# Performance work log

Hardware: AMD Instinct MI355X
Metric: run time of the kernel (lower is better)

## Reference

```python
import jax, jax.numpy as jnp
import numpy as np

PRECS = 1e-05
# HBV parameter scaling bounds (order: BETA, FC, K0, K1, K2, LP, PERC, UZL, TT, CFMAX, CFR, CWH, BETAET)
LB = jnp.array([1.0, 50.0, 0.05, 0.01, 0.001, 0.2, 0.0, 0.0, -2.5, 0.5, 0.0, 0.0, 0.3], dtype=jnp.float32)
UB = jnp.array([6.0, 1000.0, 0.9, 0.5, 0.2, 1.0, 10.0, 100.0, 2.5, 10.0, 0.1, 0.2, 5.0], dtype=jnp.float32)

NSTEP, NGRID, MU = 730, 1000, 8

def setup_inputs() -> dict:
    key = jax.random.key(0)
    k1, k2, k3, k4 = jax.random.split(key, 4)
    P = jax.random.uniform(k1, (NSTEP, NGRID), jnp.float32) * 10.0      # precip mm/day
    T = jax.random.normal(k2, (NSTEP, NGRID), jnp.float32) * 8.0 + 2.0  # temp degC
    ET = jax.random.uniform(k3, (NSTEP, NGRID), jnp.float32) * 5.0      # PET mm/day
    x = jnp.stack([P, T, ET], axis=-1)                                   # [Nstep, Ngrid, 3]
    parameters = jax.random.uniform(k4, (NSTEP, NGRID, 13, MU), jnp.float32)  # raw in [0,1]
    tdlst = jnp.arange(2, dtype=jnp.int32)  # -> param indices {12, 0} = BETAET, BETA dynamic
    return {"x": x, "parameters": parameters, "staind": NSTEP - 1, "tdlst": tdlst, "mu": MU}

def _hbv_forward(x, parameters, staind, tdlst):
    # scale raw params to physical ranges: [Nstep, Ngrid, 13, mu]
    parT = LB[None, None, :, None] + parameters * (UB - LB)[None, None, :, None]
    # static params taken from time index staind, broadcast over time
    parhbv = jnp.broadcast_to(parT[staind][None], parT.shape)
    # dynamic params: dydrop=0 -> bernoulli mask is all zeros -> comPar = dynPar
    idx = jnp.mod(jnp.asarray(tdlst) - 1, 13)
    parhbv = parhbv.at[:, :, idx, :].set(parT[:, :, idx, :])

    Ngrid = x.shape[1]
    mu = parameters.shape[-1]
    init = tuple(jnp.full((Ngrid, mu), 0.001, dtype=jnp.float32) for _ in range(5))

    def step(carry, inp):
        SP, MW, SM, SUZ, SLZ = carry
        P_, T_, ET_, par = inp              # P_/T_/ET_: [Ngrid], par: [Ngrid, 13, mu]
        P_, T_, ET_ = P_[:, None], T_[:, None], ET_[:, None]
        BETA, FC, K0, K1, K2, LP, PERCc, UZL, TT, CFMAX, CFR, CWH, BETAET = (
            par[:, i] for i in range(13))
        is_rain = (T_ >= TT).astype(jnp.float32)
        RAIN = P_ * is_rain
        SNOW = P_ * (1.0 - is_rain)
        SP = SP + SNOW
        melt = jnp.minimum(jnp.maximum(CFMAX * (T_ - TT), 0.0), SP)
        MW = MW + melt
        SP = SP - melt
        refr = jnp.minimum(jnp.maximum(CFR * CFMAX * (TT - T_), 0.0), MW)
        SP = SP + refr
        MW = MW - refr
        tosoil = jnp.maximum(MW - CWH * SP, 0.0)
        MW = MW - tosoil
        soil_wetness = jnp.clip((SM / FC) ** BETA, 0.0, 1.0)
        recharge = (RAIN + tosoil) * soil_wetness
        SM = SM + RAIN + tosoil - recharge
        excess = jnp.maximum(SM - FC, 0.0)
        SM = SM - excess
        evapfactor = jnp.clip((SM / (LP * FC)) ** BETAET, 0.0, 1.0)
        ETact = jnp.minimum(SM, ET_ * evapfactor)
        SM = jnp.maximum(SM - ETact, PRECS)
        SUZ = SUZ + recharge + excess
        PERC = jnp.minimum(SUZ, PERCc)
        SUZ = SUZ - PERC
        Q0 = K0 * jnp.maximum(SUZ - UZL, 0.0)
        SUZ = SUZ - Q0
        Q1 = K1 * SUZ
        SUZ = SUZ - Q1
        SLZ = SLZ + PERC
        Q2 = K2 * SLZ
        SLZ = SLZ - Q2
        return (SP, MW, SM, SUZ, SLZ), Q0 + Q1 + Q2

    _, Qsimmu = jax.lax.scan(step, init, (x[:, :, 0], x[:, :, 1], x[:, :, 2], parhbv))
    # muwts=None -> mean over components; routOpt=False -> Qs = Qsimave[..., None]
    return Qsimmu.mean(-1)[..., None]  # [Nstep, Ngrid, 1]

def reference(x, parameters, staind, tdlst, mu):
    return _hbv_forward(x, parameters, staind, tdlst)
```

## Files before the change

### kernel.cpp

```cpp
#include <hip/hip_runtime.h>

#define NSTEP 730
#define NGRID 1000
#define MU    8
#define NPAR  13
#define PRECS 1e-5f

#define PAR_TSTRIDE 104000u
#define PAR_GSTRIDE 104u
#define X_TSTRIDE 3000u

#define GSTEPS 10
#define NGROUP (NSTEP / GSTEPS)

constexpr float LB_[NPAR] = {1.0f, 50.0f, 0.05f, 0.01f, 0.001f, 0.2f, 0.0f,
                             0.0f, -2.5f, 0.5f, 0.0f, 0.0f, 0.3f};
constexpr float UB_[NPAR] = {6.0f, 1000.0f, 0.9f, 0.5f, 0.2f, 1.0f, 10.0f,
                             100.0f, 2.5f, 10.0f, 0.1f, 0.2f, 5.0f};

__device__ __forceinline__ float fast_rcp(float x)  { return __builtin_amdgcn_rcpf(x); }
__device__ __forceinline__ float fast_exp2(float x) { return __builtin_amdgcn_exp2f(x); }
__device__ __forceinline__ float fast_log2(float x) { return __builtin_amdgcn_logf(x); }

__device__ __forceinline__ int mod13(int v) {
    int r = v % NPAR;
    if (r < 0) r += NPAR;
    return r;
}

template <int CTRL>
__device__ __forceinline__ float dpp_xadd(float v) {
    int r = __builtin_amdgcn_update_dpp(0, __float_as_int(v), CTRL, 0xF, 0xF, true);
    return v + __int_as_float(r);
}
__device__ __forceinline__ float mu8_sum(float v) {
    v = dpp_xadd<0xB1>(v);
    v = dpp_xadd<0x4E>(v);
    int s = __builtin_amdgcn_ds_swizzle(__float_as_int(v), 0x101F);
    return v + __int_as_float(s);
}

__device__ __forceinline__ float hbv_step_core(
    float P_, float T_, float ET_,
    float BETA, float FC, float K0, float K1, float K2,
    float PERCc, float UZL, float TT, float CFMAX, float CFR, float CWH,
    float BETAET, float rcpFC, float rcpLPFC,
    float& SP, float& MW, float& SM, float& SUZ, float& SLZ)
{
    float dT    = T_ - TT;
    float RAIN  = (T_ >= TT) ? P_ : 0.f;
    float SNOW  = P_ - RAIN;
    SP += SNOW;
    float cm    = CFMAX * dT;
    float melt  = fminf(fmaxf(cm, 0.f), SP);
    MW += melt; SP -= melt;
    float refr  = fminf(fmaxf(-CFR * cm, 0.f), MW);
    SP += refr; MW -= refr;
    float tosoil = fmaxf(MW - CWH * SP, 0.f);
    MW -= tosoil;
    float soilw  = fminf(fast_exp2(BETA * fast_log2(SM * rcpFC)), 1.f);
    float rt     = RAIN + tosoil;
    float rech   = rt * soilw;
    SM += rt - rech;
    float excess = fmaxf(SM - FC, 0.f);
    SM -= excess;
    float evapf  = fminf(fast_exp2(BETAET * fast_log2(SM * rcpLPFC)), 1.f);
    float ETact  = fminf(SM, ET_ * evapf);
    SM = fmaxf(SM - ETact, PRECS);
    SUZ += rech + excess;
    float PERC = fminf(SUZ, PERCc);
    SUZ -= PERC;
    float Q0 = K0 * fmaxf(SUZ - UZL, 0.f);
    SUZ -= Q0;
    float Q1 = K1 * SUZ;
    SUZ -= Q1;
    SLZ += PERC;
    float Q2 = K2 * SLZ;
    SLZ -= Q2;
    return Q0 + Q1 + Q2;
}

__device__ __forceinline__ void hbv_fast_12_0(
    const float* __restrict__ x, const float* __restrict__ par,
    int staind, float* __restrict__ out, int g, int m)
{
    const unsigned cpar = (unsigned)g * PAR_GSTRIDE + (unsigned)m;
    const unsigned g3   = (unsigned)g * 3u;

    float fx[NPAR];
    const unsigned sbase = (unsigned)staind * PAR_TSTRIDE + cpar;
#pragma unroll
    for (int i = 0; i < NPAR; ++i)
        fx[i] = fmaf(par[sbase + (unsigned)i * 8u], UB_[i] - LB_[i], LB_[i]);
    const float FC = fx[1], K0 = fx[2], K1 = fx[3], K2 = fx[4], LP = fx[5],
                PERCc = fx[6], UZL = fx[7], TT = fx[8], CFMAX = fx[9],
                CFR = fx[10], CWH = fx[11];
    const float rcpFC   = fast_rcp(FC);
    const float rcpLPFC = fast_rcp(LP * FC);
    constexpr float lbB = LB_[0],  dvB = UB_[0]  - LB_[0];
    constexpr float lbE = LB_[12], dvE = UB_[12] - LB_[12];

    float bP[2][GSTEPS], bT[2][GSTEPS], bEv[2][GSTEPS];
    float bS0[2][GSTEPS], bS1[2][GSTEPS];
    float SP = 0.001f, MW = 0.001f, SM = 0.001f, SUZ = 0.001f, SLZ = 0.001f;

    auto load = [&](int b, int t0) {
#pragma unroll
        for (int j = 0; j < GSTEPS; ++j) {
            unsigned t  = (unsigned)(t0 + j);
            unsigned xo = t * X_TSTRIDE + g3;
            bP[b][j]  = x[xo];
            bT[b][j]  = x[xo + 1u];
            bEv[b][j] = x[xo + 2u];
            unsigned po = t * PAR_TSTRIDE + cpar;
            bS0[b][j] = par[po + 96u];
            bS1[b][j] = par[po + 0u];
        }
    };
    auto compute = [&](int b, int t0) {
        float ql[GSTEPS];
#pragma unroll
        for (int j = 0; j < GSTEPS; ++j) {
            float BETAET = fmaf(bS0[b][j], dvE, lbE);
            float BETA   = fmaf(bS1[b][j], dvB, lbB);
            ql[j] = hbv_step_core(bP[b][j], bT[b][j], bEv[b][j],
                                  BETA, FC, K0, K1, K2, PERCc, UZL, TT, CFMAX,
                                  CFR, CWH, BETAET, rcpFC, rcpLPFC,
                                  SP, MW, SM, SUZ, SLZ);
        }
#pragma unroll
        for (int j = 0; j < GSTEPS; ++j) {
            float s = mu8_sum(ql[j]);
            if (m == 0)
                out[(unsigned)(t0 + j) * (unsigned)NGRID + (unsigned)g] = s * 0.125f;
        }
    };

    load(0, 0);
    for (int gp = 0; gp < NGROUP; gp += 2) {
        if (gp + 1 < NGROUP) load(1, (gp + 1) * GSTEPS);
        compute(0, gp * GSTEPS);
        if (gp + 2 < NGROUP) load(0, (gp + 2) * GSTEPS);
        if (gp + 1 < NGROUP) compute(1, (gp + 1) * GSTEPS);
    }
}

__device__ void hbv_generic2(
    const float* __restrict__ x, const float* __restrict__ par,
    int staind, int idx0, int idx1, float* __restrict__ out, int g, int m)
{
    const unsigned cpar = (unsigned)g * PAR_GSTRIDE + (unsigned)m;
    const unsigned g3   = (unsigned)g * 3u;

    float lb0 = 0.f, dv0 = 0.f, lb1 = 0.f, dv1 = 0.f;
    float sel0[NPAR], sel1[NPAR];
#pragma unroll
    for (int i = 0; i < NPAR; ++i) {
        sel0[i] = (idx0 == i) ? 1.f : 0.f;
        sel1[i] = (idx1 == i && idx1 != idx0) ? 1.f : 0.f;
        if (idx0 == i) { lb0 = LB_[i]; dv0 = UB_[i] - LB_[i]; }
        if (idx1 == i) { lb1 = LB_[i]; dv1 = UB_[i] - LB_[i]; }
    }
    const unsigned off0 = (unsigned)idx0 * 8u, off1 = (unsigned)idx1 * 8u;

    float basep[NPAR];
    const unsigned sbase = (unsigned)staind * PAR_TSTRIDE + cpar;
#pragma unroll
    for (int i = 0; i < NPAR; ++i) {
        float fxv = fmaf(par[sbase + (unsigned)i * 8u], UB_[i] - LB_[i], LB_[i]);
        basep[i] = fxv * (1.f - sel0[i] - sel1[i]);
    }

    float bP[2][GSTEPS], bT[2][GSTEPS], bEv[2][GSTEPS];
    float bS0[2][GSTEPS], bS1[2][GSTEPS];
    float SP = 0.001f, MW = 0.001f, SM = 0.001f, SUZ = 0.001f, SLZ = 0.001f;

    auto load = [&](int b, int t0) {
#pragma unroll
        for (int j = 0; j < GSTEPS; ++j) {
            unsigned t  = (unsigned)(t0 + j);
            unsigned xo = t * X_TSTRIDE + g3;
            bP[b][j]  = x[xo];
            bT[b][j]  = x[xo + 1u];
            bEv[b][j] = x[xo + 2u];
            unsigned po = t * PAR_TSTRIDE + cpar;
            bS0[b][j] = par[po + off0];
            bS1[b][j] = par[po + off1];
        }
    };
    auto compute = [&](int b, int t0) {
        float ql[GSTEPS];
#pragma unroll
        for (int j = 0; j < GSTEPS; ++j) {
            float sv0 = fmaf(bS0[b][j], dv0, lb0);
            float sv1 = fmaf(bS1[b][j], dv1, lb1);
            float pr[NPAR];
#pragma unroll
            for (int i = 0; i < NPAR; ++i)
                pr[i] = fmaf(sel1[i], sv1, fmaf(sel0[i], sv0, basep[i]));
            float rcpFC   = fast_rcp(pr[1]);
            float rcpLPFC = fast_rcp(pr[5] * pr[1]);
            ql[j] = hbv_step_core(bP[b][j], bT[b][j], bEv[b][j],
                                  pr[0], pr[1], pr[2], pr[3], pr[4], pr[6],
                                  pr[7], pr[8], pr[9], pr[10], pr[11], pr[12],
                                  rcpFC, rcpLPFC, SP, MW, SM, SUZ, SLZ);
        }
#pragma unroll
        for (int j = 0; j < GSTEPS; ++j) {
            float s = mu8_sum(ql[j]);
            if (m == 0)
                out[(unsigned)(t0 + j) * (unsigned)NGRID + (unsigned)g] = s * 0.125f;
        }
    };

    load(0, 0);
    for (int gp = 0; gp < NGROUP; gp += 2) {
        if (gp + 1 < NGROUP) load(1, (gp + 1) * GSTEPS);
        compute(0, gp * GSTEPS);
        if (gp + 2 < NGROUP) load(0, (gp + 2) * GSTEPS);
        if (gp + 1 < NGROUP) compute(1, (gp + 1) * GSTEPS);
    }
}

__global__ __launch_bounds__(64, 1) void hbv_main(
    const float* __restrict__ x, const float* __restrict__ par,
    const int* __restrict__ staind_p, const int* __restrict__ tdlst_p,
    float* __restrict__ out)
{
    const int tid = blockIdx.x * 64 + threadIdx.x;
    const int g   = tid >> 3;
    const int m   = tid & 7;

    const int staind = __builtin_amdgcn_readfirstlane(staind_p[0]);
    const int idx0   = __builtin_amdgcn_readfirstlane(mod13(tdlst_p[0] - 1));
    const int idx1   = __builtin_amdgcn_readfirstlane(mod13(tdlst_p[1] - 1));

    if (idx0 == 12 && idx1 == 0)
        hbv_fast_12_0(x, par, staind, out, g, m);
    else
        hbv_generic2(x, par, staind, idx0, idx1, out, g, m);
}

__global__ __launch_bounds__(64, 1) void hbv_scan_generic(
    const float* __restrict__ x, const float* __restrict__ par,
    const int* __restrict__ staind_p, const int* __restrict__ tdlst_p,
    int n_td, float* __restrict__ out)
{
    const int tid = blockIdx.x * 64 + threadIdx.x;
    const int g   = tid >> 3;
    const int m   = tid & 7;
    if (g >= NGRID) return;

    const int staind    = staind_p[0];
    const unsigned cpar = (unsigned)g * PAR_GSTRIDE + (unsigned)m;
    const unsigned g3   = (unsigned)g * 3u;

    unsigned off[NPAR], st[NPAR];
#pragma unroll
    for (int i = 0; i < NPAR; ++i) {
        bool vr = false;
        for (int j = 0; j < n_td; ++j)
            if (mod13(tdlst_p[j] - 1) == i) vr = true;
        off[i] = (vr ? 0u : (unsigned)staind * PAR_TSTRIDE) + cpar + (unsigned)i * 8u;
        st[i]  = vr ? PAR_TSTRIDE : 0u;
    }

    float SP = 0.001f, MW = 0.001f, SM = 0.001f, SUZ = 0.001f, SLZ = 0.001f;
    for (int t = 0; t < NSTEP; ++t) {
        unsigned xo = (unsigned)t * X_TSTRIDE + g3;
        float P_ = x[xo], T_ = x[xo + 1u], E_ = x[xo + 2u];
        float pr[NPAR];
#pragma unroll
        for (int i = 0; i < NPAR; ++i) {
            pr[i] = fmaf(par[off[i]], UB_[i] - LB_[i], LB_[i]);
            off[i] += st[i];
        }
        float rcpFC   = fast_rcp(pr[1]);
        float rcpLPFC = fast_rcp(pr[5] * pr[1]);
        float q = hbv_step_core(P_, T_, E_, pr[0], pr[1], pr[2], pr[3], pr[4],
                                pr[6], pr[7], pr[8], pr[9], pr[10], pr[11],
                                pr[12], rcpFC, rcpLPFC, SP, MW, SM, SUZ, SLZ);
        float s = mu8_sum(q);
        if (m == 0) out[(unsigned)t * (unsigned)NGRID + (unsigned)g] = s * 0.125f;
    }
}

extern "C" void kernel_launch(void* const* d_in, const int* in_sizes, int n_in,
                              void* d_out, int out_size, void* d_ws, size_t ws_size,
                              hipStream_t stream) {
    const float* x      = (const float*)d_in[0];
    const float* par    = (const float*)d_in[1];
    const int*   staind = (const int*)d_in[2];
    const int*   tdlst  = (const int*)d_in[3];
    float*       out    = (float*)d_out;
    const int n_td = in_sizes[3];

    const int threads = NGRID * MU;
    const int block   = 64;
    const int grid    = (threads + block - 1) / block;

    if (n_td == 2)
        hbv_main<<<grid, block, 0, stream>>>(x, par, staind, tdlst, out);
    else
        hbv_scan_generic<<<grid, block, 0, stream>>>(x, par, staind, tdlst,
                                                     n_td, out);
}
```

Before: 469.7 us.

## Triple-buffer loads and hoist off-chain work out of the HBV recurrence

Rewrites the fast path for dynamic params {12,0} to triple-buffer the per-step loads in groups of 5 steps, keeping two groups of loads in flight instead of one. Work that does not depend on the state (rain/snow split, melt and refreeze caps, parameter scaling, and the log2(1/FC) terms folded into the power exponents) moves into a pre-pass, shortening the serial dependency chain. It also fuses several ops with fma and drops a clip. The goal is to hide memory latency and cut per-step latency on the recurrence, at the cost of more registers and small floating-point differences.

```diff
diff --git a/kernel.cpp b/kernel.cpp
--- a/kernel.cpp
+++ b/kernel.cpp
@@ -13,6 +13,9 @@
 #define GSTEPS 10
 #define NGROUP (NSTEP / GSTEPS)
 
+#define G5  5
+#define NG5 (NSTEP / G5)
+
 constexpr float LB_[NPAR] = {1.0f, 50.0f, 0.05f, 0.01f, 0.001f, 0.2f, 0.0f,
                              0.0f, -2.5f, 0.5f, 0.0f, 0.0f, 0.3f};
 constexpr float UB_[NPAR] = {6.0f, 1000.0f, 0.9f, 0.5f, 0.2f, 1.0f, 10.0f,
@@ -38,6 +41,118 @@
     v = dpp_xadd<0x4E>(v);
     int s = __builtin_amdgcn_ds_swizzle(__float_as_int(v), 0x101F);
     return v + __int_as_float(s);
+}
+
+__device__ __forceinline__ void hbv_fast_12_0(
+    const float* __restrict__ x, const float* __restrict__ par,
+    int staind, float* __restrict__ out, int g, int m)
+{
+    const unsigned cpar = (unsigned)g * PAR_GSTRIDE + (unsigned)m;
+    const unsigned g3   = (unsigned)g * 3u;
+
+    float fx[NPAR];
+    const unsigned sbase = (unsigned)staind * PAR_TSTRIDE + cpar;
+#pragma unroll
+    for (int i = 0; i < NPAR; ++i)
+        fx[i] = fmaf(par[sbase + (unsigned)i * 8u], UB_[i] - LB_[i], LB_[i]);
+    const float FC = fx[1], K0 = fx[2], K1 = fx[3], K2 = fx[4], LP = fx[5],
+                PERCc = fx[6], UZL = fx[7], TT = fx[8], CFMAX = fx[9],
+                CFR = fx[10], CWH = fx[11];
+    const float rcpFC    = fast_rcp(FC);
+    const float rcpLPFC  = fast_rcp(LP * FC);
+    const float l2rcpFC  = fast_log2(rcpFC);
+    const float l2rcpLPF = fast_log2(rcpLPFC);
+    const float CC       = CFR * CFMAX;
+    constexpr float lbB = LB_[0],  dvB = UB_[0]  - LB_[0];
+    constexpr float lbE = LB_[12], dvE = UB_[12] - LB_[12];
+
+    float bP[3][G5], bT[3][G5], bE[3][G5], b0[3][G5], b1[3][G5];
+    float SP = 0.001f, MW = 0.001f, SM = 0.001f, SUZ = 0.001f, SLZ = 0.001f;
+
+    auto load = [&](int b, int t0) {
+#pragma unroll
+        for (int j = 0; j < G5; ++j) {
+            unsigned t  = (unsigned)(t0 + j);
+            unsigned xo = t * X_TSTRIDE + g3;
+            bP[b][j] = x[xo];
+            bT[b][j] = x[xo + 1u];
+            bE[b][j] = x[xo + 2u];
+            unsigned po = t * PAR_TSTRIDE + cpar;
+            b0[b][j] = par[po + 96u];
+            b1[b][j] = par[po + 0u];
+        }
+    };
+
+    auto compute = [&](int b, int t0) {
+        float RAINv[G5], SNOWv[G5], MAXCM[G5], MAXRF[G5], ETv[G5];
+        float BETAv[G5], BETEv[G5], bbc[G5], ebc[G5];
+#pragma unroll
+        for (int j = 0; j < G5; ++j) {
+            float Pj = bP[b][j], Tj = bT[b][j];
+            float dT = Tj - TT;
+            float RAIN = (dT >= 0.f) ? Pj : 0.f;
+            RAINv[j] = RAIN;
+            SNOWv[j] = Pj - RAIN;
+            float cm = CFMAX * dT;
+            MAXCM[j] = fmaxf(cm, 0.f);
+            MAXRF[j] = fmaxf(-CC * dT, 0.f);
+            ETv[j]   = bE[b][j];
+            float BETAET = fmaf(b0[b][j], dvE, lbE);
+            float BETA   = fmaf(b1[b][j], dvB, lbB);
+            BETAv[j] = BETA;  BETEv[j] = BETAET;
+            bbc[j] = BETA   * l2rcpFC;
+            ebc[j] = BETAET * l2rcpLPF;
+        }
+        float ql[G5];
+#pragma unroll
+        for (int j = 0; j < G5; ++j) {
+            SP += SNOWv[j];
+            float melt = fminf(MAXCM[j], SP);
+            MW += melt; SP -= melt;
+            float refr = fminf(MAXRF[j], MW);
+            SP += refr; MW -= refr;
+            float tosoil = fmaxf(fmaf(-CWH, SP, MW), 0.f);
+            MW -= tosoil;
+            float rt   = RAINv[j] + tosoil;
+            float smrt = SM + rt;
+            float soilw = fast_exp2(fmaf(BETAv[j], fast_log2(SM), bbc[j]));
+            float rech  = rt * soilw;
+            float SM_mid = smrt - rech;
+            float SM_ae  = fminf(SM_mid, FC);
+            float excess = SM_mid - SM_ae;
+            float evapf  = fminf(fast_exp2(fmaf(BETEv[j], fast_log2(SM_ae), ebc[j])), 1.f);
+            SM = fmaxf(fmaf(-ETv[j], evapf, SM_ae), PRECS);
+            SUZ += rech + excess;
+            float PERC = fminf(SUZ, PERCc);
+            float SUZp = SUZ - PERC;
+            float Q0   = K0 * fmaxf(SUZp - UZL, 0.f);
+            float SUZq = SUZp - Q0;
+            float Q1   = K1 * SUZq;
+            SUZ = SUZq - Q1;
+            SLZ += PERC;
+            float Q2 = K2 * SLZ;
+            SLZ -= Q2;
+            ql[j] = (Q0 + Q1) + Q2;
+        }
+#pragma unroll
+        for (int j = 0; j < G5; ++j) ql[j] = mu8_sum(ql[j]);
+        if (m == 0) {
+#pragma unroll
+            for (int j = 0; j < G5; ++j)
+                out[(unsigned)(t0 + j) * (unsigned)NGRID + (unsigned)g] = ql[j] * 0.125f;
+        }
+    };
+
+    load(0, 0);
+    load(1, G5);
+    int grp = 0;
+    for (int it = 0; it < 48; ++it, grp += 3) {
+        load(2, (grp + 2) * G5); compute(0, grp * G5);
+        load(0, (grp + 3) * G5); compute(1, (grp + 1) * G5);
+        load(1, (grp + 4) * G5); compute(2, (grp + 2) * G5);
+    }
+    compute(0, 144 * G5);
+    compute(1, 145 * G5);
 }
 
 __device__ __forceinline__ float hbv_step_core(
@@ -80,71 +195,6 @@
     return Q0 + Q1 + Q2;
 }
 
-__device__ __forceinline__ void hbv_fast_12_0(
-    const float* __restrict__ x, const float* __restrict__ par,
-    int staind, float* __restrict__ out, int g, int m)
-{
-    const unsigned cpar = (unsigned)g * PAR_GSTRIDE + (unsigned)m;
-    const unsigned g3   = (unsigned)g * 3u;
-
-    float fx[NPAR];
-    const unsigned sbase = (unsigned)staind * PAR_TSTRIDE + cpar;
-#pragma unroll
-    for (int i = 0; i < NPAR; ++i)
-        fx[i] = fmaf(par[sbase + (unsigned)i * 8u], UB_[i] - LB_[i], LB_[i]);
-    const float FC = fx[1], K0 = fx[2], K1 = fx[3], K2 = fx[4], LP = fx[5],
-                PERCc = fx[6], UZL = fx[7], TT = fx[8], CFMAX = fx[9],
-                CFR = fx[10], CWH = fx[11];
-    const float rcpFC   = fast_rcp(FC);
-    const float rcpLPFC = fast_rcp(LP * FC);
-    constexpr float lbB = LB_[0],  dvB = UB_[0]  - LB_[0];
-    constexpr float lbE = LB_[12], dvE = UB_[12] - LB_[12];
-
-    float bP[2][GSTEPS], bT[2][GSTEPS], bEv[2][GSTEPS];
-    float bS0[2][GSTEPS], bS1[2][GSTEPS];
-    float SP = 0.001f, MW = 0.001f, SM = 0.001f, SUZ = 0.001f, SLZ = 0.001f;
-
-    auto load = [&](int b, int t0) {
-#pragma unroll
-        for (int j = 0; j < GSTEPS; ++j) {
-            unsigned t  = (unsigned)(t0 + j);
-            unsigned xo = t * X_TSTRIDE + g3;
-            bP[b][j]  = x[xo];
-            bT[b][j]  = x[xo + 1u];
-            bEv[b][j] = x[xo + 2u];
-            unsigned po = t * PAR_TSTRIDE + cpar;
-            bS0[b][j] = par[po + 96u];
-            bS1[b][j] = par[po + 0u];
-        }
-    };
-    auto compute = [&](int b, int t0) {
-        float ql[GSTEPS];
-#pragma unroll
-        for (int j = 0; j < GSTEPS; ++j) {
-            float BETAET = fmaf(bS0[b][j], dvE, lbE);
-            float BETA   = fmaf(bS1[b][j], dvB, lbB);
-            ql[j] = hbv_step_core(bP[b][j], bT[b][j], bEv[b][j],
-                                  BETA, FC, K0, K1, K2, PERCc, UZL, TT, CFMAX,
-                                  CFR, CWH, BETAET, rcpFC, rcpLPFC,
-                                  SP, MW, SM, SUZ, SLZ);
-        }
-#pragma unroll
-        for (int j = 0; j < GSTEPS; ++j) {
-            float s = mu8_sum(ql[j]);
-            if (m == 0)
-                out[(unsigned)(t0 + j) * (unsigned)NGRID + (unsigned)g] = s * 0.125f;
-        }
-    };
-
-    load(0, 0);
-    for (int gp = 0; gp < NGROUP; gp += 2) {
-        if (gp + 1 < NGROUP) load(1, (gp + 1) * GSTEPS);
-        compute(0, gp * GSTEPS);
-        if (gp + 2 < NGROUP) load(0, (gp + 2) * GSTEPS);
-        if (gp + 1 < NGROUP) compute(1, (gp + 1) * GSTEPS);
-    }
-}
-
 __device__ void hbv_generic2(
     const float* __restrict__ x, const float* __restrict__ par,
     int staind, int idx0, int idx1, float* __restrict__ out, int g, int m)
```

Result: faster. 430.9 us (-8.3%).
